# Kernel optimization log

Measured on AMD Instinct MI355X. Metric: run time of the kernel, lower is better.

The kernel has to match this reference:

```python
import jax, jax.numpy as jnp
import numpy as np

B, CDD, L, T, H, NH = 16, 10, 64, 128, 768, 12
DH = H // NH          # head dim = 64
S = CDD * L + T       # full sequence = 768 (640 candidate tokens + 128 terms)


def setup_inputs() -> dict:
    key = jax.random.key(0)
    ks = jax.random.split(key, 7)
    w = 0.02
    return {
        "hidden_states": jax.random.normal(ks[0], (B, S, H), jnp.float32),
        "Wq": jax.random.normal(ks[1], (H, H), jnp.float32) * w,
        "bq": jax.random.normal(ks[2], (H,), jnp.float32) * w,
        "Wk": jax.random.normal(ks[3], (H, H), jnp.float32) * w,
        "bk": jax.random.normal(ks[4], (H,), jnp.float32) * w,
        "Wv": jax.random.normal(ks[5], (H, H), jnp.float32) * w,
        "bv": jax.random.normal(ks[6], (H,), jnp.float32) * w,
    }


def _one_pass_mask(dtype):
    # block-diagonal over candidates + dense global columns for terms
    block = jnp.kron(jnp.eye(CDD, dtype=dtype), jnp.ones((L, L), dtype=dtype))  # [CDD*L, CDD*L]
    return jnp.concatenate([block, jnp.ones((CDD * L, T), dtype=dtype)], axis=-1)  # [CDD*L, S]


def reference(hidden_states, Wq, bq, Wk, bk, Wv, bv):
    def split_heads(x):  # [B, s, H] -> [B, NH, s, DH]
        return x.reshape(B, -1, NH, DH).transpose(0, 2, 1, 3)

    attn_field = hidden_states[:, :-T]                     # [B, CDD*L, H] queries only
    q = split_heads(attn_field @ Wq.T + bq)                # [B, NH, CDD*L, DH]
    k = split_heads(hidden_states @ Wk.T + bk)             # [B, NH, S, DH]
    v = split_heads(hidden_states @ Wv.T + bv)             # [B, NH, S, DH]

    mask = _one_pass_mask(q.dtype)                         # [CDD*L, S]
    scale = 1.0 / np.sqrt(DH).astype(np.float32)
    # NOTE: original multiplies scores by the mask (masked entries become 0, not -inf)
    scores = jnp.einsum('bhqd,bhkd->bhqk', q, k) * scale * mask
    probs = jax.nn.softmax(scores, axis=-1)                # [B, NH, CDD*L, S]

    ctx = jnp.einsum('bhqk,bhkd->bhqd', probs, v)          # [B, NH, CDD*L, DH]
    ctx = jnp.concatenate([ctx, v[:, :, -T:]], axis=2)     # append term values untouched
    return ctx.transpose(0, 2, 1, 3).reshape(B, S, H)
```

## Files before the change

### kernel.cpp

```cpp
#include <hip/hip_runtime.h>

constexpr int Bb  = 16;
constexpr int CDD = 10;
constexpr int Lc  = 64;
constexpr int T   = 128;
constexpr int H   = 768;
constexpr int NH  = 12;
constexpr int DH  = 64;
constexpr int S   = 768;
constexpr int SQ  = 640;
constexpr int MROWS = Bb * S;

typedef __attribute__((ext_vector_type(8))) short bf16x8;
typedef __attribute__((ext_vector_type(4))) short bf16x4;
typedef __attribute__((ext_vector_type(4))) float f32x4;

__device__ inline unsigned short f2bf(float f) {
  unsigned u = __float_as_uint(f);
  u += 0x7fff + ((u >> 16) & 1);
  return (unsigned short)(u >> 16);
}
__device__ inline float bf2f(unsigned short h) {
  return __uint_as_float(((unsigned)h) << 16);
}

__device__ inline void gld_lds16(const void* g, void* l) {
  __builtin_amdgcn_global_load_lds(
      (const __attribute__((address_space(1))) void*)g,
      (__attribute__((address_space(3))) void*)l, 16, 0, 0);
}

__device__ inline bf16x8 ld_b64x2(const unsigned short* p) {
  union { bf16x8 v; bf16x4 h[2]; } u;
  u.h[0] = *(const bf16x4*)p;
  u.h[1] = *(const bf16x4*)(p + 4);
  return u.v;
}

constexpr int NX4 = MROWS * H / 4;
constexpr int NW4 = H * H / 4;
__global__ void convert_all(const float* __restrict__ X,
                            const float* __restrict__ Wq,
                            const float* __restrict__ Wk,
                            const float* __restrict__ Wv,
                            unsigned short* __restrict__ Xb,
                            unsigned short* __restrict__ Wb) {
  int i = blockIdx.x * blockDim.x + threadIdx.x;
  const int stride = gridDim.x * blockDim.x;
  const int total = NX4 + 3 * NW4;
  for (; i < total; i += stride) {
    const float* src;
    unsigned short* dst;
    int off;
    if (i < NX4) {
      src = X; dst = Xb; off = i;
    } else {
      int k = i - NX4;
      int w = k / NW4;
      off = k - w * NW4;
      src = (w == 0) ? Wq : (w == 1) ? Wk : Wv;
      dst = Wb + (size_t)w * H * H;
    }
    float4 v = ((const float4*)src)[i < NX4 ? off : off];
    ushort4 o;
    o.x = f2bf(v.x); o.y = f2bf(v.y); o.z = f2bf(v.z); o.w = f2bf(v.w);
    ((ushort4*)dst)[off] = o;
  }
}

__launch_bounds__(256, 4)
__global__ void qkv_gemm(const unsigned short* __restrict__ Xb,
                         const unsigned short* __restrict__ Wb,
                         const float* __restrict__ bq, const float* __restrict__ bk,
                         const float* __restrict__ bv,
                         unsigned short* __restrict__ Qb, unsigned short* __restrict__ Kb,
                         unsigned short* __restrict__ Vb,
                         float* __restrict__ part,
                         float* __restrict__ out) {
  const int z = blockIdx.z;
  if (z == 0 && (blockIdx.x % 6) == 5) return;
  const unsigned short* W = Wb + (size_t)z * H * H;
  const float* bias = (z == 0) ? bq : (z == 1) ? bk : bv;
  unsigned short* Y = (z == 0) ? Qb : (z == 1) ? Kb : Vb;

  const int i0 = blockIdx.x * 128;
  const int j0 = blockIdx.y * 128;
  const int tid = threadIdx.x;
  const int wave = tid >> 6, lane = tid & 63;
  const int wr = wave >> 1, wc = wave & 1;
  const int col = lane & 15, quad = lane >> 4;

  __shared__ unsigned short As[128 * 64];
  __shared__ unsigned short Bs[128 * 64];

  f32x4 acc[4][4];
#pragma unroll
  for (int i = 0; i < 4; i++)
#pragma unroll
    for (int j = 0; j < 4; j++) acc[i][j] = (f32x4){0.f, 0.f, 0.f, 0.f};

  int rS[4], gcS[4];
#pragma unroll
  for (int i = 0; i < 4; i++) {
    int s = tid + 256 * i;
    rS[i] = s >> 3;
    gcS[i] = (s & 7) ^ (rS[i] & 7);
  }

  for (int kt = 0; kt < 12; kt++) {
    const int k0 = kt * 64;
#pragma unroll
    for (int i = 0; i < 4; i++)
      gld_lds16(Xb + (size_t)(i0 + rS[i]) * H + k0 + gcS[i] * 8, &As[(tid + 256 * i) * 8]);
#pragma unroll
    for (int i = 0; i < 4; i++)
      gld_lds16(W + (size_t)(j0 + rS[i]) * H + k0 + gcS[i] * 8, &Bs[(tid + 256 * i) * 8]);
    __builtin_amdgcn_s_waitcnt(0);
    __syncthreads();

#pragma unroll
    for (int h = 0; h < 2; h++) {
      bf16x8 a[4], b[4];
#pragma unroll
      for (int mt = 0; mt < 4; mt++) {
        int r = wr * 64 + mt * 16 + col;
        a[mt] = *(const bf16x8*)&As[r * 64 + (((h * 4 + quad) ^ (r & 7)) * 8)];
      }
#pragma unroll
      for (int nt = 0; nt < 4; nt++) {
        int r = wc * 64 + nt * 16 + col;
        b[nt] = *(const bf16x8*)&Bs[r * 64 + (((h * 4 + quad) ^ (r & 7)) * 8)];
      }
#pragma unroll
      for (int mt = 0; mt < 4; mt++)
#pragma unroll
        for (int nt = 0; nt < 4; nt++)
          acc[mt][nt] = __builtin_amdgcn_mfma_f32_16x16x32_bf16(a[mt], b[nt], acc[mt][nt], 0, 0, 0);
    }
    __syncthreads();
  }

  float colsum[4] = {0.f, 0.f, 0.f, 0.f};
#pragma unroll
  for (int mt = 0; mt < 4; mt++) {
#pragma unroll
    for (int nt = 0; nt < 4; nt++) {
      const int j = j0 + wc * 64 + nt * 16 + col;
      const float bj = bias[j];
#pragma unroll
      for (int r = 0; r < 4; r++) {
        const int i = i0 + wr * 64 + mt * 16 + quad * 4 + r;
        const float v = acc[mt][nt][r] + bj;
        Y[(size_t)i * H + j] = f2bf(v);
        if (z == 2) {
          colsum[nt] += v;
          int s = i - (i / S) * S;
          if (s >= SQ) out[(size_t)i * H + j] = v;
        }
      }
    }
  }
  if (z == 2) {
    const int b = blockIdx.x / 6;
#pragma unroll
    for (int nt = 0; nt < 4; nt++) {
      float s = colsum[nt];
      s += __shfl_xor(s, 16, 64);
      s += __shfl_xor(s, 32, 64);
      if (quad == 0) {
        const int j = j0 + wc * 64 + nt * 16 + col;
        atomicAdd(&part[b * H + j], s);
      }
    }
  }
}

__launch_bounds__(256, 2)
__global__ void attn_kernel(const unsigned short* __restrict__ Qb,
                            const unsigned short* __restrict__ Kb,
                            const unsigned short* __restrict__ Vb,
                            const float* __restrict__ part,
                            float* __restrict__ out) {
  const int bid = blockIdx.x;
  const int c = bid % CDD;
  const int h = (bid / CDD) % NH;
  const int b = bid / (CDD * NH);
  const int tid = threadIdx.x;
  const int wave = tid >> 6, lane = tid & 63;
  const int col = lane & 15, quad = lane >> 4;

  __shared__ __align__(16) char smem[59136];
  unsigned short* Qs = (unsigned short*)smem;
  unsigned short* Ks = (unsigned short*)(smem + 8192);
  unsigned short* Ps = (unsigned short*)smem;
  unsigned short* Vt = (unsigned short*)(smem + 32768);
  float* red   = (float*)(smem + 57856);
  float* vcorr = (float*)(smem + 58880);

  const size_t rowQ0 = (size_t)(b * S + c * 64) * H + h * DH;

  {
    int s0 = tid, s1 = tid + 256;
    int r0 = s0 >> 3, g0 = (s0 & 7) ^ (r0 & 7);
    int r1 = s1 >> 3, g1 = (s1 & 7) ^ (r1 & 7);
    gld_lds16(Qb + rowQ0 + (size_t)r0 * H + g0 * 8, &Qs[s0 * 8]);
    gld_lds16(Qb + rowQ0 + (size_t)r1 * H + g1 * 8, &Qs[s1 * 8]);
  }
#pragma unroll
  for (int j = 0; j < 6; j++) {
    int s = tid + 256 * j;
    int key = s >> 3;
    int gkey = (key < 64) ? (c * 64 + key) : (576 + key);
    int gc = (s & 7) ^ (key & 7);
    gld_lds16(Kb + (size_t)(b * S + gkey) * H + h * DH + gc * 8, &Ks[s * 8]);
  }
#pragma unroll
  for (int j = 0; j < 6; j++) {
    int s = tid + 256 * j;
    int key = s >> 3;
    int f0 = (s & 7) * 8;
    int gkey = (key < 64) ? (c * 64 + key) : (576 + key);
    union { int4 i4; unsigned short u[8]; } uv;
    uv.i4 = *(const int4*)(Vb + (size_t)(b * S + gkey) * H + h * DH + f0);
#pragma unroll
    for (int i = 0; i < 8; i++) Vt[(f0 + i) * 196 + key] = uv.u[i];
  }
  __builtin_amdgcn_s_waitcnt(0);
  __syncthreads();

  {
    int d = tid & 63, p = tid >> 6;
    float sum = 0.f;
    for (int k = p * 48; k < p * 48 + 48; k++) sum += bf2f(Vt[d * 196 + k]);
    red[tid] = sum;
  }
  __syncthreads();
  if (tid < 64) {
    float tot = part[b * H + h * DH + tid];
    vcorr[tid] = tot - (red[tid] + red[64 + tid] + red[128 + tid] + red[192 + tid]);
  }

  f32x4 sc[12];
#pragma unroll
  for (int n = 0; n < 12; n++) sc[n] = (f32x4){0.f, 0.f, 0.f, 0.f};
  {
    const int rq = wave * 16 + col;
    bf16x8 a0 = *(const bf16x8*)&Qs[rq * 64 + ((quad ^ (rq & 7)) * 8)];
    bf16x8 a1 = *(const bf16x8*)&Qs[rq * 64 + (((4 + quad) ^ (rq & 7)) * 8)];
#pragma unroll
    for (int n = 0; n < 12; n++) {
      const int rk = n * 16 + col;
      bf16x8 b0 = *(const bf16x8*)&Ks[rk * 64 + ((quad ^ (rk & 7)) * 8)];
      bf16x8 b1 = *(const bf16x8*)&Ks[rk * 64 + (((4 + quad) ^ (rk & 7)) * 8)];
      sc[n] = __builtin_amdgcn_mfma_f32_16x16x32_bf16(a0, b0, sc[n], 0, 0, 0);
      sc[n] = __builtin_amdgcn_mfma_f32_16x16x32_bf16(a1, b1, sc[n], 0, 0, 0);
    }
  }

  float em[4], zin[4];
  {
    const float scale = 0.125f;
#pragma unroll
    for (int r = 0; r < 4; r++) {
      float mx = sc[0][r];
#pragma unroll
      for (int n = 1; n < 12; n++) mx = fmaxf(mx, sc[n][r]);
#pragma unroll
      for (int msk = 1; msk <= 8; msk <<= 1) mx = fmaxf(mx, __shfl_xor(mx, msk, 64));
      const float mrow = fmaxf(mx * scale, 0.f);
      float rs = 0.f;
#pragma unroll
      for (int n = 0; n < 12; n++) {
        float p = __expf(sc[n][r] * scale - mrow);
        sc[n][r] = p;
        rs += p;
      }
#pragma unroll
      for (int msk = 1; msk <= 8; msk <<= 1) rs += __shfl_xor(rs, msk, 64);
      const float e = __expf(-mrow);
      em[r] = e;
      zin[r] = 1.f / (rs + 576.f * e);
    }
  }
  __syncthreads();

#pragma unroll
  for (int n = 0; n < 12; n++)
#pragma unroll
    for (int r = 0; r < 4; r++)
      Ps[(wave * 16 + quad * 4 + r) * 196 + n * 16 + col] = f2bf(sc[n][r]);
  __syncthreads();

  f32x4 o[4];
#pragma unroll
  for (int n2 = 0; n2 < 4; n2++) o[n2] = (f32x4){0.f, 0.f, 0.f, 0.f};
#pragma unroll
  for (int ks = 0; ks < 6; ks++) {
    bf16x8 a = ld_b64x2(&Ps[(wave * 16 + col) * 196 + ks * 32 + quad * 8]);
#pragma unroll
    for (int n2 = 0; n2 < 4; n2++) {
      bf16x8 bvv = ld_b64x2(&Vt[(n2 * 16 + col) * 196 + ks * 32 + quad * 8]);
      o[n2] = __builtin_amdgcn_mfma_f32_16x16x32_bf16(a, bvv, o[n2], 0, 0, 0);
    }
  }

#pragma unroll
  for (int n2 = 0; n2 < 4; n2++) {
    const int d = n2 * 16 + col;
    const float vc = vcorr[d];
#pragma unroll
    for (int r = 0; r < 4; r++) {
      const int m = wave * 16 + quad * 4 + r;
      const float val = (o[n2][r] + em[r] * vc) * zin[r];
      out[(size_t)(b * S + c * 64 + m) * H + h * DH + d] = val;
    }
  }
}

extern "C" void kernel_launch(void* const* d_in, const int* in_sizes, int n_in,
                              void* d_out, int out_size, void* d_ws, size_t ws_size,
                              hipStream_t stream) {
  const float* X  = (const float*)d_in[0];
  const float* Wq = (const float*)d_in[1];
  const float* bq = (const float*)d_in[2];
  const float* Wk = (const float*)d_in[3];
  const float* bk = (const float*)d_in[4];
  const float* Wv = (const float*)d_in[5];
  const float* bv = (const float*)d_in[6];
  float* out = (float*)d_out;

  char* ws = (char*)d_ws;
  unsigned short* Xb   = (unsigned short*)ws;
  unsigned short* Wb   = (unsigned short*)(ws + 18874368);
  unsigned short* Qb   = (unsigned short*)(ws + 22413312);
  unsigned short* Kb   = (unsigned short*)(ws + 41287680);
  unsigned short* Vb   = (unsigned short*)(ws + 60162048);
  float*          part = (float*)(ws + 79036416);

  hipMemsetAsync(part, 0, Bb * H * sizeof(float), stream);
  convert_all<<<2048, 256, 0, stream>>>(X, Wq, Wk, Wv, Xb, Wb);
  qkv_gemm<<<dim3(96, 6, 3), 256, 0, stream>>>(Xb, Wb, bq, bk, bv, Qb, Kb, Vb, part, out);
  attn_kernel<<<1920, 256, 0, stream>>>(Qb, Kb, Vb, part, out);
}
```

Measured before the change: 180.1 us.

## Enlarge QKV GEMM tiles to 256x256 with double-buffered LDS prefetch

Restructures the QKV projection GEMM to use 512-thread blocks computing 256x256 output tiles. Next-k-tile global-to-LDS loads are double-buffered and interleaved with the MFMA work, and MFMA sections run at raised wave priority. Waves covering unused Q rows (the term tokens) skip their compute instead of returning whole blocks. The grid drops to 432 blocks and LDS use rises to 128KB per block, which lowers occupancy and may leave CUs underfilled.

```diff
diff --git a/kernel.cpp b/kernel.cpp
--- a/kernel.cpp
+++ b/kernel.cpp
@@ -61,14 +61,14 @@
       src = (w == 0) ? Wq : (w == 1) ? Wk : Wv;
       dst = Wb + (size_t)w * H * H;
     }
-    float4 v = ((const float4*)src)[i < NX4 ? off : off];
+    float4 v = ((const float4*)src)[off];
     ushort4 o;
     o.x = f2bf(v.x); o.y = f2bf(v.y); o.z = f2bf(v.z); o.w = f2bf(v.w);
     ((ushort4*)dst)[off] = o;
   }
 }
 
-__launch_bounds__(256, 4)
+__launch_bounds__(512, 2)
 __global__ void qkv_gemm(const unsigned short* __restrict__ Xb,
                          const unsigned short* __restrict__ Wb,
                          const float* __restrict__ bq, const float* __restrict__ bk,
@@ -77,99 +77,134 @@
                          unsigned short* __restrict__ Vb,
                          float* __restrict__ part,
                          float* __restrict__ out) {
-  const int z = blockIdx.z;
-  if (z == 0 && (blockIdx.x % 6) == 5) return;
+  const int z  = blockIdx.y / 3;
+  const int j0 = (blockIdx.y % 3) * 256;
+  const int i0 = blockIdx.x * 256;
+  const int xb3 = blockIdx.x % 3;
   const unsigned short* W = Wb + (size_t)z * H * H;
   const float* bias = (z == 0) ? bq : (z == 1) ? bk : bv;
   unsigned short* Y = (z == 0) ? Qb : (z == 1) ? Kb : Vb;
 
-  const int i0 = blockIdx.x * 128;
-  const int j0 = blockIdx.y * 128;
   const int tid = threadIdx.x;
   const int wave = tid >> 6, lane = tid & 63;
-  const int wr = wave >> 1, wc = wave & 1;
+  const int wr = wave >> 2, wc = wave & 3;
   const int col = lane & 15, quad = lane >> 4;
 
-  __shared__ unsigned short As[128 * 64];
-  __shared__ unsigned short Bs[128 * 64];
-
-  f32x4 acc[4][4];
-#pragma unroll
-  for (int i = 0; i < 4; i++)
+  const bool skipC = (z == 0) && (xb3 == 2) && (wr == 1);
+
+  __shared__ unsigned short As0[256 * 64];
+  __shared__ unsigned short As1[256 * 64];
+  __shared__ unsigned short Bs0[256 * 64];
+  __shared__ unsigned short Bs1[256 * 64];
+
+  f32x4 acc[8][4];
+#pragma unroll
+  for (int i = 0; i < 8; i++)
 #pragma unroll
     for (int j = 0; j < 4; j++) acc[i][j] = (f32x4){0.f, 0.f, 0.f, 0.f};
 
   int rS[4], gcS[4];
 #pragma unroll
   for (int i = 0; i < 4; i++) {
-    int s = tid + 256 * i;
+    int s = tid + 512 * i;
     rS[i] = s >> 3;
     gcS[i] = (s & 7) ^ (rS[i] & 7);
   }
 
+#pragma unroll
+  for (int i = 0; i < 4; i++) {
+    gld_lds16(Xb + (size_t)(i0 + rS[i]) * H + gcS[i] * 8, &As0[(tid + 512 * i) * 8]);
+    gld_lds16(W  + (size_t)(j0 + rS[i]) * H + gcS[i] * 8, &Bs0[(tid + 512 * i) * 8]);
+  }
+  __builtin_amdgcn_s_waitcnt(0);
+  __syncthreads();
+
+  bf16x8 bfr[2][4];
+
   for (int kt = 0; kt < 12; kt++) {
-    const int k0 = kt * 64;
-#pragma unroll
-    for (int i = 0; i < 4; i++)
-      gld_lds16(Xb + (size_t)(i0 + rS[i]) * H + k0 + gcS[i] * 8, &As[(tid + 256 * i) * 8]);
-#pragma unroll
-    for (int i = 0; i < 4; i++)
-      gld_lds16(W + (size_t)(j0 + rS[i]) * H + k0 + gcS[i] * 8, &Bs[(tid + 256 * i) * 8]);
-    __builtin_amdgcn_s_waitcnt(0);
-    __syncthreads();
-
-#pragma unroll
-    for (int h = 0; h < 2; h++) {
-      bf16x8 a[4], b[4];
-#pragma unroll
-      for (int mt = 0; mt < 4; mt++) {
-        int r = wr * 64 + mt * 16 + col;
-        a[mt] = *(const bf16x8*)&As[r * 64 + (((h * 4 + quad) ^ (r & 7)) * 8)];
-      }
+    const unsigned short* Ar = (kt & 1) ? As1 : As0;
+    const unsigned short* Br = (kt & 1) ? Bs1 : Bs0;
+    unsigned short* Aw = (kt & 1) ? As0 : As1;
+    unsigned short* Bw = (kt & 1) ? Bs0 : Bs1;
+    const int k0n = (kt + 1) * 64;
+    const bool pf = (kt < 11);
+
+#pragma unroll
+    for (int p = 0; p < 4; p++) {
+      if (pf && p < 2) {
+#pragma unroll
+        for (int q2 = 0; q2 < 2; q2++) {
+          const int i = p * 2 + q2;
+          gld_lds16(Xb + (size_t)(i0 + rS[i]) * H + k0n + gcS[i] * 8,
+                    &Aw[(tid + 512 * i) * 8]);
+          gld_lds16(W  + (size_t)(j0 + rS[i]) * H + k0n + gcS[i] * 8,
+                    &Bw[(tid + 512 * i) * 8]);
+        }
+      }
+      const int mh = p >> 1, h = p & 1;
+      if (!skipC) {
+        bf16x8 a[4];
+#pragma unroll
+        for (int mt = 0; mt < 4; mt++) {
+          const int r = wr * 128 + (mh * 4 + mt) * 16 + col;
+          a[mt] = *(const bf16x8*)&Ar[r * 64 + (((h * 4 + quad) ^ (r & 7)) * 8)];
+        }
+        if (mh == 0) {
+#pragma unroll
+          for (int nt = 0; nt < 4; nt++) {
+            const int rB = wc * 64 + nt * 16 + col;
+            bfr[h][nt] = *(const bf16x8*)&Br[rB * 64 + (((h * 4 + quad) ^ (rB & 7)) * 8)];
+          }
+        }
+        __builtin_amdgcn_s_setprio(1);
+#pragma unroll
+        for (int mt = 0; mt < 4; mt++)
+#pragma unroll
+          for (int nt = 0; nt < 4; nt++)
+            acc[mh * 4 + mt][nt] = __builtin_amdgcn_mfma_f32_16x16x32_bf16(
+                a[mt], bfr[h][nt], acc[mh * 4 + mt][nt], 0, 0, 0);
+        __builtin_amdgcn_s_setprio(0);
+      }
+    }
+    if (pf) {
+      __builtin_amdgcn_s_waitcnt(0);
+      __syncthreads();
+    }
+  }
+
+  if (!skipC) {
+    const int sbase = xb3 * 256 + wr * 128;
+    float colsum[4] = {0.f, 0.f, 0.f, 0.f};
+#pragma unroll
+    for (int mf = 0; mf < 8; mf++) {
 #pragma unroll
       for (int nt = 0; nt < 4; nt++) {
-        int r = wc * 64 + nt * 16 + col;
-        b[nt] = *(const bf16x8*)&Bs[r * 64 + (((h * 4 + quad) ^ (r & 7)) * 8)];
-      }
-#pragma unroll
-      for (int mt = 0; mt < 4; mt++)
-#pragma unroll
-        for (int nt = 0; nt < 4; nt++)
-          acc[mt][nt] = __builtin_amdgcn_mfma_f32_16x16x32_bf16(a[mt], b[nt], acc[mt][nt], 0, 0, 0);
-    }
-    __syncthreads();
-  }
-
-  float colsum[4] = {0.f, 0.f, 0.f, 0.f};
-#pragma unroll
-  for (int mt = 0; mt < 4; mt++) {
-#pragma unroll
-    for (int nt = 0; nt < 4; nt++) {
-      const int j = j0 + wc * 64 + nt * 16 + col;
-      const float bj = bias[j];
-#pragma unroll
-      for (int r = 0; r < 4; r++) {
-        const int i = i0 + wr * 64 + mt * 16 + quad * 4 + r;
-        const float v = acc[mt][nt][r] + bj;
-        Y[(size_t)i * H + j] = f2bf(v);
-        if (z == 2) {
-          colsum[nt] += v;
-          int s = i - (i / S) * S;
-          if (s >= SQ) out[(size_t)i * H + j] = v;
-        }
-      }
-    }
-  }
-  if (z == 2) {
-    const int b = blockIdx.x / 6;
-#pragma unroll
-    for (int nt = 0; nt < 4; nt++) {
-      float s = colsum[nt];
-      s += __shfl_xor(s, 16, 64);
-      s += __shfl_xor(s, 32, 64);
-      if (quad == 0) {
         const int j = j0 + wc * 64 + nt * 16 + col;
-        atomicAdd(&part[b * H + j], s);
+        const float bj = bias[j];
+#pragma unroll
+        for (int r = 0; r < 4; r++) {
+          const int i = i0 + wr * 128 + mf * 16 + quad * 4 + r;
+          const float v = acc[mf][nt][r] + bj;
+          Y[(size_t)i * H + j] = f2bf(v);
+          if (z == 2) {
+            colsum[nt] += v;
+            const int s = sbase + mf * 16 + quad * 4 + r;
+            if (s >= SQ) out[(size_t)i * H + j] = v;
+          }
+        }
+      }
+    }
+    if (z == 2) {
+      const int b = blockIdx.x / 3;
+#pragma unroll
+      for (int nt = 0; nt < 4; nt++) {
+        float s = colsum[nt];
+        s += __shfl_xor(s, 16, 64);
+        s += __shfl_xor(s, 32, 64);
+        if (quad == 0) {
+          const int j = j0 + wc * 64 + nt * 16 + col;
+          atomicAdd(&part[b * H + j], s);
+        }
       }
     }
   }
@@ -339,6 +374,6 @@
 
   hipMemsetAsync(part, 0, Bb * H * sizeof(float), stream);
   convert_all<<<2048, 256, 0, stream>>>(X, Wq, Wk, Wv, Xb, Wb);
-  qkv_gemm<<<dim3(96, 6, 3), 256, 0, stream>>>(Xb, Wb, bq, bk, bv, Qb, Kb, Vb, part, out);
+  qkv_gemm<<<dim3(48, 9), 512, 0, stream>>>(Xb, Wb, bq, bk, bv, Qb, Kb, Vb, part, out);
   attn_kernel<<<1920, 256, 0, stream>>>(Qb, Kb, Vb, part, out);
 }
```

Result: no change. 180.6 us (+0.3%).

## Rewrite QKV GEMM as 256x256 tiles with double-buffered LDS and interleaved staging

Applied to the files above, without the earlier changes.

The QKV projection GEMM moves from 128x128 tiles with 256 threads to 256x256 tiles with 512 threads. LDS is double-buffered and the next k-slice is loaded in quarters, interleaved with four MFMA phases and gated by vmcnt waits and barriers. MFMA sections run at raised wave priority. The aim is to hide global-to-LDS latency and increase data reuse per tile, at the cost of 128KB of LDS per block, lower occupancy, and a coarse 432-block grid. Q tiles that fall entirely in the term rows are still partly skipped.

```diff
diff --git a/kernel.cpp b/kernel.cpp
--- a/kernel.cpp
+++ b/kernel.cpp
@@ -61,14 +61,14 @@
       src = (w == 0) ? Wq : (w == 1) ? Wk : Wv;
       dst = Wb + (size_t)w * H * H;
     }
-    float4 v = ((const float4*)src)[i < NX4 ? off : off];
+    float4 v = ((const float4*)src)[off];
     ushort4 o;
     o.x = f2bf(v.x); o.y = f2bf(v.y); o.z = f2bf(v.z); o.w = f2bf(v.w);
     ((ushort4*)dst)[off] = o;
   }
 }
 
-__launch_bounds__(256, 4)
+__launch_bounds__(512, 2)
 __global__ void qkv_gemm(const unsigned short* __restrict__ Xb,
                          const unsigned short* __restrict__ Wb,
                          const float* __restrict__ bq, const float* __restrict__ bk,
@@ -77,102 +77,185 @@
                          unsigned short* __restrict__ Vb,
                          float* __restrict__ part,
                          float* __restrict__ out) {
-  const int z = blockIdx.z;
-  if (z == 0 && (blockIdx.x % 6) == 5) return;
+  const int z  = blockIdx.y / 3;
+  const int j0 = (blockIdx.y % 3) * 256;
+  const int i0 = blockIdx.x * 256;
+  const int xb3 = blockIdx.x % 3;
   const unsigned short* W = Wb + (size_t)z * H * H;
   const float* bias = (z == 0) ? bq : (z == 1) ? bk : bv;
   unsigned short* Y = (z == 0) ? Qb : (z == 1) ? Kb : Vb;
 
-  const int i0 = blockIdx.x * 128;
-  const int j0 = blockIdx.y * 128;
   const int tid = threadIdx.x;
   const int wave = tid >> 6, lane = tid & 63;
-  const int wr = wave >> 1, wc = wave & 1;
+  const int wr = wave >> 2, wc = wave & 3;
   const int col = lane & 15, quad = lane >> 4;
 
-  __shared__ unsigned short As[128 * 64];
-  __shared__ unsigned short Bs[128 * 64];
-
-  f32x4 acc[4][4];
-#pragma unroll
-  for (int i = 0; i < 4; i++)
+  const bool skipHi = (z == 0) && (xb3 == 2);
+
+  __shared__ unsigned short As0[256 * 64];
+  __shared__ unsigned short As1[256 * 64];
+  __shared__ unsigned short Bs0[256 * 64];
+  __shared__ unsigned short Bs1[256 * 64];
+
+  f32x4 acc[8][4];
+#pragma unroll
+  for (int i = 0; i < 8; i++)
 #pragma unroll
     for (int j = 0; j < 4; j++) acc[i][j] = (f32x4){0.f, 0.f, 0.f, 0.f};
 
-  int rS[4], gcS[4];
-#pragma unroll
-  for (int i = 0; i < 4; i++) {
-    int s = tid + 256 * i;
-    rS[i] = s >> 3;
-    gcS[i] = (s & 7) ^ (rS[i] & 7);
-  }
-
-  for (int kt = 0; kt < 12; kt++) {
-    const int k0 = kt * 64;
-#pragma unroll
-    for (int i = 0; i < 4; i++)
-      gld_lds16(Xb + (size_t)(i0 + rS[i]) * H + k0 + gcS[i] * 8, &As[(tid + 256 * i) * 8]);
-#pragma unroll
-    for (int i = 0; i < 4; i++)
-      gld_lds16(W + (size_t)(j0 + rS[i]) * H + k0 + gcS[i] * 8, &Bs[(tid + 256 * i) * 8]);
-    __builtin_amdgcn_s_waitcnt(0);
-    __syncthreads();
-
-#pragma unroll
-    for (int h = 0; h < 2; h++) {
-      bf16x8 a[4], b[4];
-#pragma unroll
-      for (int mt = 0; mt < 4; mt++) {
-        int r = wr * 64 + mt * 16 + col;
-        a[mt] = *(const bf16x8*)&As[r * 64 + (((h * 4 + quad) ^ (r & 7)) * 8)];
-      }
-#pragma unroll
-      for (int nt = 0; nt < 4; nt++) {
-        int r = wc * 64 + nt * 16 + col;
-        b[nt] = *(const bf16x8*)&Bs[r * 64 + (((h * 4 + quad) ^ (r & 7)) * 8)];
-      }
-#pragma unroll
-      for (int mt = 0; mt < 4; mt++)
-#pragma unroll
-        for (int nt = 0; nt < 4; nt++)
-          acc[mt][nt] = __builtin_amdgcn_mfma_f32_16x16x32_bf16(a[mt], b[nt], acc[mt][nt], 0, 0, 0);
-    }
-    __syncthreads();
-  }
-
+  bf16x8 a[4][2];
+  bf16x8 b[2][2][2];
+
+#define STAGE_HALF(src, dst, rowbase, k0, hf)                                   \
+  do {                                                                          \
+    _Pragma("unroll") for (int u = 0; u < 2; u++) {                             \
+      const int s_ = tid + 512 * u;                                             \
+      const int r_ = (s_ >> 3) + (hf) * 128;                                    \
+      const int c_ = s_ & 7;                                                    \
+      gld_lds16((src) + (size_t)((rowbase) + r_) * H + (k0) + ((c_ ^ (r_ & 7)) * 8), \
+                &(dst)[(r_ * 8 + c_) * 8]);                                     \
+    }                                                                           \
+  } while (0)
+
+#define READ_A(mh_)                                                             \
+  do {                                                                          \
+    _Pragma("unroll") for (int mt = 0; mt < 4; mt++) {                          \
+      const int r_ = (mh_) * 128 + wr * 64 + mt * 16 + col;                     \
+      _Pragma("unroll") for (int kh = 0; kh < 2; kh++)                          \
+        a[mt][kh] = *(const bf16x8*)&Ar[r_ * 64 + (((kh * 4 + quad) ^ (r_ & 7)) * 8)]; \
+    }                                                                           \
+  } while (0)
+
+#define READ_B(nh_)                                                             \
+  do {                                                                          \
+    _Pragma("unroll") for (int nf = 0; nf < 2; nf++) {                          \
+      const int r_ = (nh_) * 128 + wc * 32 + nf * 16 + col;                     \
+      _Pragma("unroll") for (int kh = 0; kh < 2; kh++)                          \
+        b[nh_][nf][kh] = *(const bf16x8*)&Br[r_ * 64 + (((kh * 4 + quad) ^ (r_ & 7)) * 8)]; \
+    }                                                                           \
+  } while (0)
+
+#define MFMA16(mh_, nh_)                                                        \
+  do {                                                                          \
+    __builtin_amdgcn_s_setprio(1);                                              \
+    _Pragma("unroll") for (int mt = 0; mt < 4; mt++)                            \
+      _Pragma("unroll") for (int nf = 0; nf < 2; nf++)                          \
+        _Pragma("unroll") for (int kh = 0; kh < 2; kh++)                        \
+          acc[(mh_) * 4 + mt][(nh_) * 2 + nf] =                                 \
+              __builtin_amdgcn_mfma_f32_16x16x32_bf16(                          \
+                  a[mt][kh], b[nh_][nf][kh], acc[(mh_) * 4 + mt][(nh_) * 2 + nf], 0, 0, 0); \
+    __builtin_amdgcn_s_setprio(0);                                              \
+  } while (0)
+
+#define GATE4 asm volatile("s_waitcnt vmcnt(4)" ::: "memory")
+#define GATE2 asm volatile("s_waitcnt vmcnt(2)" ::: "memory")
+#define GATE0 asm volatile("s_waitcnt vmcnt(0)" ::: "memory")
+#define BAR                                                                     \
+  do {                                                                          \
+    asm volatile("" ::: "memory");                                              \
+    __builtin_amdgcn_s_barrier();                                               \
+    asm volatile("" ::: "memory");                                              \
+  } while (0)
+
+  STAGE_HALF(Xb, As0, i0, 0, 0);
+  STAGE_HALF(W,  Bs0, j0, 0, 0);
+  STAGE_HALF(W,  Bs0, j0, 0, 1);
+  STAGE_HALF(Xb, As0, i0, 0, 1);
+  GATE0;
+  BAR;
+
+  for (int t = 0; t < 11; t++) {
+    const unsigned short* Ar = (t & 1) ? As1 : As0;
+    const unsigned short* Br = (t & 1) ? Bs1 : Bs0;
+    unsigned short* Aw = (t & 1) ? As0 : As1;
+    unsigned short* Bw = (t & 1) ? Bs0 : Bs1;
+    const int k0n = (t + 1) * 64;
+
+    READ_A(0); READ_B(0);
+    STAGE_HALF(Xb, Aw, i0, k0n, 0);
+    GATE4; BAR;
+    MFMA16(0, 0);
+    BAR;
+
+    READ_B(1);
+    STAGE_HALF(W, Bw, j0, k0n, 0);
+    GATE4; BAR;
+    MFMA16(0, 1);
+    BAR;
+
+    if (!skipHi) READ_A(1);
+    STAGE_HALF(W, Bw, j0, k0n, 1);
+    BAR;
+    if (!skipHi) MFMA16(1, 0);
+    BAR;
+
+    STAGE_HALF(Xb, Aw, i0, k0n, 1);
+    GATE4; BAR;
+    if (!skipHi) MFMA16(1, 1);
+    BAR;
+  }
+
+  {
+    const unsigned short* Ar = As1;
+    const unsigned short* Br = Bs1;
+    READ_A(0); READ_B(0);
+    GATE2; BAR;
+    MFMA16(0, 0);
+    BAR;
+    READ_B(1);
+    GATE0; BAR;
+    MFMA16(0, 1);
+    if (!skipHi) {
+      READ_A(1);
+      MFMA16(1, 0);
+      MFMA16(1, 1);
+    }
+  }
+
+  const int b_ = blockIdx.x / 3;
   float colsum[4] = {0.f, 0.f, 0.f, 0.f};
 #pragma unroll
-  for (int mt = 0; mt < 4; mt++) {
-#pragma unroll
-    for (int nt = 0; nt < 4; nt++) {
-      const int j = j0 + wc * 64 + nt * 16 + col;
+  for (int mf = 0; mf < 8; mf++) {
+    if (skipHi && mf >= 4) continue;
+    const int rloc = (mf >> 2) * 128 + wr * 64 + (mf & 3) * 16;
+#pragma unroll
+    for (int nf = 0; nf < 4; nf++) {
+      const int j = j0 + (nf >> 1) * 128 + wc * 32 + (nf & 1) * 16 + col;
       const float bj = bias[j];
 #pragma unroll
       for (int r = 0; r < 4; r++) {
-        const int i = i0 + wr * 64 + mt * 16 + quad * 4 + r;
-        const float v = acc[mt][nt][r] + bj;
+        const int iloc = rloc + quad * 4 + r;
+        const int i = i0 + iloc;
+        const float v = acc[mf][nf][r] + bj;
         Y[(size_t)i * H + j] = f2bf(v);
         if (z == 2) {
-          colsum[nt] += v;
-          int s = i - (i / S) * S;
+          colsum[nf] += v;
+          const int s = xb3 * 256 + iloc;
           if (s >= SQ) out[(size_t)i * H + j] = v;
         }
       }
     }
   }
   if (z == 2) {
-    const int b = blockIdx.x / 6;
-#pragma unroll
-    for (int nt = 0; nt < 4; nt++) {
-      float s = colsum[nt];
+#pragma unroll
+    for (int nf = 0; nf < 4; nf++) {
+      float s = colsum[nf];
       s += __shfl_xor(s, 16, 64);
       s += __shfl_xor(s, 32, 64);
       if (quad == 0) {
-        const int j = j0 + wc * 64 + nt * 16 + col;
-        atomicAdd(&part[b * H + j], s);
+        const int j = j0 + (nf >> 1) * 128 + wc * 32 + (nf & 1) * 16 + col;
+        atomicAdd(&part[b_ * H + j], s);
       }
     }
   }
+#undef STAGE_HALF
+#undef READ_A
+#undef READ_B
+#undef MFMA16
+#undef GATE4
+#undef GATE2
+#undef GATE0
+#undef BAR
 }
 
 __launch_bounds__(256, 2)
@@ -339,6 +422,6 @@
 
   hipMemsetAsync(part, 0, Bb * H * sizeof(float), stream);
   convert_all<<<2048, 256, 0, stream>>>(X, Wq, Wk, Wv, Xb, Wb);
-  qkv_gemm<<<dim3(96, 6, 3), 256, 0, stream>>>(Xb, Wb, bq, bk, bv, Qb, Kb, Vb, part, out);
+  qkv_gemm<<<dim3(48, 9), 512, 0, stream>>>(Xb, Wb, bq, bk, bv, Qb, Kb, Vb, part, out);
   attn_kernel<<<1920, 256, 0, stream>>>(Qb, Kb, Vb, part, out);
 }
```

New measurement: 187.5 us. 4.1% more time.

## Defer V transpose into LDS and compute V column sums with MFMA

Applied to the files above, without the earlier changes.

V tiles are now loaded into registers and written transposed into LDS only after the QK^T and softmax phase, so global V latency overlaps with score computation. A partial waitcnt lets the Q/K async loads complete without waiting on the V loads. The separate LDS reduction of V column sums, with its two extra barriers, is replaced by an MFMA against a ones vector that runs alongside the PV product, which frees the reduction scratch LDS. The cost is more live registers across softmax and double the MFMA count in the PV loop.

```diff
diff --git a/kernel.cpp b/kernel.cpp
--- a/kernel.cpp
+++ b/kernel.cpp
@@ -61,7 +61,7 @@
       src = (w == 0) ? Wq : (w == 1) ? Wk : Wv;
       dst = Wb + (size_t)w * H * H;
     }
-    float4 v = ((const float4*)src)[i < NX4 ? off : off];
+    float4 v = ((const float4*)src)[off];
     ushort4 o;
     o.x = f2bf(v.x); o.y = f2bf(v.y); o.z = f2bf(v.z); o.w = f2bf(v.w);
     ((ushort4*)dst)[off] = o;
@@ -189,13 +189,11 @@
   const int wave = tid >> 6, lane = tid & 63;
   const int col = lane & 15, quad = lane >> 4;
 
-  __shared__ __align__(16) char smem[59136];
+  __shared__ __align__(16) char smem[57856];
   unsigned short* Qs = (unsigned short*)smem;
   unsigned short* Ks = (unsigned short*)(smem + 8192);
   unsigned short* Ps = (unsigned short*)smem;
   unsigned short* Vt = (unsigned short*)(smem + 32768);
-  float* red   = (float*)(smem + 57856);
-  float* vcorr = (float*)(smem + 58880);
 
   const size_t rowQ0 = (size_t)(b * S + c * 64) * H + h * DH;
 
@@ -214,31 +212,21 @@
     int gc = (s & 7) ^ (key & 7);
     gld_lds16(Kb + (size_t)(b * S + gkey) * H + h * DH + gc * 8, &Ks[s * 8]);
   }
+  asm volatile("" ::: "memory");
+
+  int4 uv[6];
 #pragma unroll
   for (int j = 0; j < 6; j++) {
     int s = tid + 256 * j;
     int key = s >> 3;
     int f0 = (s & 7) * 8;
     int gkey = (key < 64) ? (c * 64 + key) : (576 + key);
-    union { int4 i4; unsigned short u[8]; } uv;
-    uv.i4 = *(const int4*)(Vb + (size_t)(b * S + gkey) * H + h * DH + f0);
-#pragma unroll
-    for (int i = 0; i < 8; i++) Vt[(f0 + i) * 196 + key] = uv.u[i];
-  }
-  __builtin_amdgcn_s_waitcnt(0);
-  __syncthreads();
-
-  {
-    int d = tid & 63, p = tid >> 6;
-    float sum = 0.f;
-    for (int k = p * 48; k < p * 48 + 48; k++) sum += bf2f(Vt[d * 196 + k]);
-    red[tid] = sum;
-  }
-  __syncthreads();
-  if (tid < 64) {
-    float tot = part[b * H + h * DH + tid];
-    vcorr[tid] = tot - (red[tid] + red[64 + tid] + red[128 + tid] + red[192 + tid]);
-  }
+    uv[j] = *(const int4*)(Vb + (size_t)(b * S + gkey) * H + h * DH + f0);
+  }
+  asm volatile("s_waitcnt vmcnt(6)" ::: "memory");
+  __builtin_amdgcn_sched_barrier(0);
+  __builtin_amdgcn_s_barrier();
+  __builtin_amdgcn_sched_barrier(0);
 
   f32x4 sc[12];
 #pragma unroll
@@ -289,11 +277,28 @@
 #pragma unroll
     for (int r = 0; r < 4; r++)
       Ps[(wave * 16 + quad * 4 + r) * 196 + n * 16 + col] = f2bf(sc[n][r]);
+
+#pragma unroll
+  for (int j = 0; j < 6; j++) {
+    int s = tid + 256 * j;
+    int key = s >> 3;
+    int f0 = (s & 7) * 8;
+    union { int4 i4; unsigned short u[8]; } w;
+    w.i4 = uv[j];
+#pragma unroll
+    for (int i = 0; i < 8; i++) Vt[(f0 + i) * 196 + key] = w.u[i];
+  }
   __syncthreads();
 
-  f32x4 o[4];
-#pragma unroll
-  for (int n2 = 0; n2 < 4; n2++) o[n2] = (f32x4){0.f, 0.f, 0.f, 0.f};
+  f32x4 o[4], osum[4];
+#pragma unroll
+  for (int n2 = 0; n2 < 4; n2++) {
+    o[n2] = (f32x4){0.f, 0.f, 0.f, 0.f};
+    osum[n2] = (f32x4){0.f, 0.f, 0.f, 0.f};
+  }
+  bf16x8 ones;
+#pragma unroll
+  for (int i = 0; i < 8; i++) ones[i] = (short)0x3F80;
 #pragma unroll
   for (int ks = 0; ks < 6; ks++) {
     bf16x8 a = ld_b64x2(&Ps[(wave * 16 + col) * 196 + ks * 32 + quad * 8]);
@@ -301,13 +306,14 @@
     for (int n2 = 0; n2 < 4; n2++) {
       bf16x8 bvv = ld_b64x2(&Vt[(n2 * 16 + col) * 196 + ks * 32 + quad * 8]);
       o[n2] = __builtin_amdgcn_mfma_f32_16x16x32_bf16(a, bvv, o[n2], 0, 0, 0);
+      osum[n2] = __builtin_amdgcn_mfma_f32_16x16x32_bf16(ones, bvv, osum[n2], 0, 0, 0);
     }
   }
 
 #pragma unroll
   for (int n2 = 0; n2 < 4; n2++) {
     const int d = n2 * 16 + col;
-    const float vc = vcorr[d];
+    const float vc = part[b * H + h * DH + d] - osum[n2][0];
 #pragma unroll
     for (int r = 0; r < 4; r++) {
       const int m = wave * 16 + quad * 4 + r;
```

Result: no change. 178.6 us (-0.9%).
